# Performance work log

Hardware: AMD Instinct MI355X
Metric: run time of the kernel (lower is better)

The kernel has to match this reference:

```python
import jax, jax.numpy as jnp
import numpy as np

NUM_CLASSES = 20
MEM_SIZE = 512      # memory_bank_size
MAX_VIEWS = 512
TEMP = 0.1
MOMENTUM = 0.999
IGNORE_IDX = 255
AUX_IDX = 254
EPS = 1e-12


def _nearest_resize(gt, Ho, Wo):
    # torch F.interpolate(mode='nearest'): src = floor(dst * in/out)
    B, Hi, Wi = gt.shape
    ri = (jnp.arange(Ho) * Hi) // Ho
    ci = (jnp.arange(Wo) * Wi) // Wo
    return gt[:, ri][:, :, ci]


def _norm_flat(p):
    # L2-normalize over channels, then [B, C, H, W] -> [B, H*W, C]
    p = p / jnp.maximum(jnp.linalg.norm(p, axis=1, keepdims=True), EPS)
    B, C = p.shape[0], p.shape[1]
    return p.reshape(B, C, -1).transpose(0, 2, 1)


def setup_inputs() -> dict:
    key = jax.random.key(0)
    k1, k2, k3, k4, k5 = jax.random.split(key, 5)
    B, D, H, W = 4, 256, 128, 128
    Hg, Wg = 512, 512
    return {
        'main_proj': jax.random.normal(k1, (B, D, H, W), dtype=jnp.float32),
        'main_gt': jax.random.randint(k2, (B, Hg, Wg), 0, NUM_CLASSES).astype(jnp.int64),
        'aux_proj': jax.random.normal(k3, (B, D, H, W), dtype=jnp.float32),
        'aux_gt': jax.random.randint(k4, (B, Hg, Wg), 0, NUM_CLASSES).astype(jnp.int64),
        'memory_bank': jax.random.normal(k5, (NUM_CLASSES, MEM_SIZE, D), dtype=jnp.float32),
    }


def reference(main_proj, main_gt, aux_proj, aux_gt, memory_bank):
    C, M, D = memory_bank.shape
    B, _, H, W = main_proj.shape
    mg = _nearest_resize(main_gt, H, W)
    ag = _nearest_resize(aux_gt, aux_proj.shape[2], aux_proj.shape[3])

    embd = jnp.concatenate([_norm_flat(main_proj), _norm_flat(aux_proj)], axis=1)
    embd = embd.reshape(-1, D)                       # [N, D]
    label = jnp.concatenate([mg.reshape(B, -1), ag.reshape(B, -1)], axis=1).reshape(-1)

    valid = label != IGNORE_IDX
    label = jnp.where(label == AUX_IDX, C - 1, label)

    # per-class gather: stable argsort puts class-c pixels first (deterministic
    # stand-in for torch.randperm selection)
    masks = (label[None, :] == jnp.arange(C)[:, None]) & valid[None, :]   # [C, N]
    counts = masks.sum(axis=1)                                           # [C]
    order = jnp.argsort(~masks, axis=1, stable=True)[:, :M]              # [C, M]
    sel = embd[order]                                                    # [C, M, D]
    sel_valid = jnp.arange(M)[None, :] < counts[:, None]                 # [C, M]

    # momentum scatter-update to memory bank (no grad through features)
    upd = MOMENTUM * memory_bank + (1.0 - MOMENTUM) * jax.lax.stop_gradient(sel)
    upd = upd / jnp.maximum(jnp.linalg.norm(upd, axis=2, keepdims=True), EPS)
    bank = jnp.where(sel_valid[..., None], upd, memory_bank)             # [C, M, D]

    # anchors from current batch (with grad)
    V = min(MAX_VIEWS, M)
    anchors = sel[:, :V].reshape(C * V, D)
    a_valid = sel_valid[:, :V].reshape(-1)
    a_lbl = jnp.repeat(jnp.arange(C), V)

    # contrastive samples from updated bank (constant w.r.t. grad)
    contras = bank.reshape(C * M, D)
    c_valid = jnp.linalg.norm(bank, axis=2).reshape(-1) > 0
    c_lbl = jnp.repeat(jnp.arange(C), M)

    # InfoNCE with masked softmax over valid contrastive columns
    scores = (anchors @ contras.T) / TEMP                                # [A, K]
    scores = jnp.where(c_valid[None, :], scores, -1e9)
    logp = jax.nn.log_softmax(scores, axis=1)
    pos = ((a_lbl[:, None] == c_lbl[None, :]) & c_valid[None, :]).astype(scores.dtype)
    pos_sum = (pos * logp).sum(axis=1)
    pos_cnt = pos.sum(axis=1)
    va = (pos_cnt > 0) & a_valid
    mlpp = jnp.where(va, pos_sum / jnp.maximum(pos_cnt, 1.0), 0.0)
    loss = -mlpp.sum() / jnp.maximum(va.sum(), 1).astype(scores.dtype)
    return loss
```

## Files before the change

### kernel.cpp

```cpp
#include <hip/hip_runtime.h>
#include <cstdint>
#include <math.h>

#define NCLS  20
#define MSZ   512
#define DIM   256
#define HW    16384
#define NPIX  131072
#define AROWS 10240
#define TEMP_INV 10.0f
#define EXP2K 14.4269504088896f

typedef __attribute__((ext_vector_type(8))) short bf16x8;
typedef __attribute__((ext_vector_type(4))) float f32x4;

__device__ __forceinline__ short f2bf(float f) {
    unsigned u = __float_as_uint(f);
    unsigned r = (u + 0x7FFFu + ((u >> 16) & 1u)) >> 16;
    return (short)r;
}
__device__ __forceinline__ float bf2f(short s) {
    return __uint_as_float(((unsigned)(unsigned short)s) << 16);
}
__device__ __forceinline__ float fexp2(float x) {
    float r;
    asm volatile("v_exp_f32 %0, %1" : "=v"(r) : "v"(x));
    return r;
}
__device__ __forceinline__ void gld16(const void* g, void* l) {
    __builtin_amdgcn_global_load_lds(
        (const __attribute__((address_space(1))) unsigned int*)(uintptr_t)g,
        (__attribute__((address_space(3))) unsigned int*)(unsigned int)(uintptr_t)l,
        16, 0, 0);
}

#define ZREG_FLOATS 15488

__global__ __launch_bounds__(256) void k_hist(const int* __restrict__ mg,
                                              const int* __restrict__ ag,
                                              int* __restrict__ labels,
                                              int* __restrict__ hist,
                                              int* __restrict__ pix2row,
                                              float* __restrict__ zreg) {
    int chunk = blockIdx.x, t = threadIdx.x;
    int lane = t & 63;
    int gi = chunk * 256 + t;
    if (gi < ZREG_FLOATS) zreg[gi] = 0.0f;

    int n = gi;
    int b = n >> 15, r = n & 32767;
    const int* g = (r < HW) ? mg : ag;
    int p = (r < HW) ? r : (r - HW);
    int h = p >> 7, w = p & 127;
    int lab = g[(((size_t)b * 512) + (size_t)(h << 2)) * 512 + (size_t)(w << 2)];
    if (lab == 255) lab = -1;
    else if (lab == 254) lab = NCLS - 1;
    labels[n] = lab;
    pix2row[n] = -1;

    __shared__ int cnt20[NCLS];
    if (t < NCLS) cnt20[t] = 0;
    __syncthreads();
#pragma unroll
    for (int c = 0; c < NCLS; ++c) {
        unsigned long long m = __ballot(lab == c);
        if (lane == 0 && m) atomicAdd(&cnt20[c], __popcll(m));
    }
    __syncthreads();
    if (t < NCLS) hist[t * 512 + chunk] = cnt20[t];
}

__global__ __launch_bounds__(256) void k_write(const int* __restrict__ labels,
                                               const int* __restrict__ hist,
                                               int* __restrict__ pix2row,
                                               int* __restrict__ counts) {
    int chunk = blockIdx.x, t = threadIdx.x;
    int lane = t & 63, wv = t >> 6;
    __shared__ int cbase[NCLS];
    __shared__ int wcnt2[4][NCLS];

#pragma unroll
    for (int cc = 0; cc < 5; ++cc) {
        int c = wv * 5 + cc;
        int s = 0;
        for (int j = lane; j < chunk; j += 64) s += hist[c * 512 + j];
#pragma unroll
        for (int o = 32; o > 0; o >>= 1) s += __shfl_down(s, o, 64);
        if (lane == 0) cbase[c] = s;
    }

    int n = chunk * 256 + t;
    int lab = labels[n];
    int myrank = 0;
#pragma unroll
    for (int c = 0; c < NCLS; ++c) {
        unsigned long long m = __ballot(lab == c);
        if (lane == 0) wcnt2[wv][c] = __popcll(m);
        if (lab == c) myrank = __popcll(m & ((1ull << lane) - 1ull));
    }
    __syncthreads();
    if (lab >= 0) {
        int base = cbase[lab] + myrank;
        for (int w = 0; w < wv; ++w) base += wcnt2[w][lab];
        if (base < MSZ) pix2row[n] = lab * MSZ + base;
    }
    if (chunk == 511 && t < NCLS)
        counts[t] = cbase[t] + wcnt2[0][t] + wcnt2[1][t] + wcnt2[2][t] + wcnt2[3][t];
}

__global__ __launch_bounds__(256) void k_scatter(const float* __restrict__ mainp,
                                                 const float* __restrict__ auxp,
                                                 const int* __restrict__ pix2row,
                                                 float* __restrict__ xF) {
    int idx = blockIdx.x * 256 + threadIdx.x;
    int p4 = idx & 4095;
    int ch = (idx >> 12) & 255;
    int bs = idx >> 20;
    int b = bs >> 1, src = bs & 1;
    const float* base = (src ? auxp : mainp) + (size_t)b * DIM * HW + (size_t)ch * HW;
    float4 v = *(const float4*)(base + p4 * 4);
    int4 pr = *(const int4*)(pix2row + bs * HW + p4 * 4);
    if (pr.x >= 0) xF[(size_t)pr.x * DIM + ch] = v.x;
    if (pr.y >= 0) xF[(size_t)pr.y * DIM + ch] = v.y;
    if (pr.z >= 0) xF[(size_t)pr.z * DIM + ch] = v.z;
    if (pr.w >= 0) xF[(size_t)pr.w * DIM + ch] = v.w;
}

__global__ __launch_bounds__(256) void k_nbc(const float* __restrict__ xF,
                                             const float* __restrict__ bank,
                                             const int* __restrict__ counts,
                                             short* __restrict__ anchorsB,
                                             short* __restrict__ contrasB,
                                             int* __restrict__ c_valid,
                                             float* __restrict__ S,
                                             int* __restrict__ pcnt) {
    int blk = blockIdx.x;
    int c = blk >> 3;
    int t = threadIdx.x, lane = t & 63, wv = t >> 6;
    int cc = counts[c];
    int base = blk * 64;
    float sacc[4] = {0.f, 0.f, 0.f, 0.f};
    int vcnt = 0;

    for (int it = 0; it < 16; ++it) {
        int a = base + it * 4 + wv;
        int m = a & 511;
        float4 xv = *(const float4*)&xF[(size_t)a * DIM + lane * 4];
        float x[4] = {xv.x, xv.y, xv.z, xv.w};
        float ss = x[0]*x[0] + x[1]*x[1] + x[2]*x[2] + x[3]*x[3];
#pragma unroll
        for (int o = 1; o < 64; o <<= 1) ss += __shfl_xor(ss, o, 64);
        float scale = 1.0f / fmaxf(sqrtf(ss), 1e-12f);
        float ax[4];
#pragma unroll
        for (int q = 0; q < 4; ++q) ax[q] = x[q] * scale;
        short4 oa;
        oa.x = f2bf(ax[0]); oa.y = f2bf(ax[1]); oa.z = f2bf(ax[2]); oa.w = f2bf(ax[3]);
        *(short4*)&anchorsB[(size_t)a * DIM + lane * 4] = oa;

        bool upd = m < cc;
        float4 bv = *(const float4*)&bank[(size_t)a * DIM + lane * 4];
        float u[4];
        u[0] = upd ? 0.999f * bv.x + 0.001f * ax[0] : bv.x;
        u[1] = upd ? 0.999f * bv.y + 0.001f * ax[1] : bv.y;
        u[2] = upd ? 0.999f * bv.z + 0.001f * ax[2] : bv.z;
        u[3] = upd ? 0.999f * bv.w + 0.001f * ax[3] : bv.w;
        float ss2 = u[0]*u[0] + u[1]*u[1] + u[2]*u[2] + u[3]*u[3];
#pragma unroll
        for (int o = 1; o < 64; o <<= 1) ss2 += __shfl_xor(ss2, o, 64);
        float nrm = sqrtf(ss2);
        float inv = 1.0f / fmaxf(nrm, 1e-12f);
        short oc[4];
        oc[0] = f2bf(upd ? u[0] * inv : bv.x);
        oc[1] = f2bf(upd ? u[1] * inv : bv.y);
        oc[2] = f2bf(upd ? u[2] * inv : bv.z);
        oc[3] = f2bf(upd ? u[3] * inv : bv.w);
        *(short4*)&contrasB[(size_t)a * DIM + lane * 4] = *(short4*)oc;
        bool valid = nrm > 0.0f;
        if (lane == 0) {
            c_valid[a] = valid ? 1 : 0;
            vcnt += valid ? 1 : 0;
        }
        if (valid) {
#pragma unroll
            for (int q = 0; q < 4; ++q) sacc[q] += bf2f(oc[q]);
        }
    }

    __shared__ float s4[4][DIM];
    __shared__ int pv[4];
#pragma unroll
    for (int q = 0; q < 4; ++q) s4[wv][lane * 4 + q] = sacc[q];
    if (lane == 0) pv[wv] = vcnt;
    __syncthreads();
    float s = s4[0][t] + s4[1][t] + s4[2][t] + s4[3][t];
    atomicAdd(&S[c * DIM + t], s);
    if (t == 0) atomicAdd(&pcnt[c], pv[0] + pv[1] + pv[2] + pv[3]);
}

__global__ __launch_bounds__(512, 4) void k_score(const short* __restrict__ A,
                                                  const short* __restrict__ Bc,
                                                  const int* __restrict__ c_valid,
                                                  float* __restrict__ row_sumexp) {
    __shared__ short As[2][128 * 32];
    __shared__ short Bs[2][256 * 32];
    int t = threadIdx.x;
    int lane = t & 63, wv = t >> 6;
    int wr = wv & 1, wc = wv >> 1;
    int row0 = blockIdx.x * 128, col0 = blockIdx.y * 256;
    int lrow = lane >> 2;
    int gseg = (lane & 3) ^ (lrow & 3);
    int qr = lane >> 4, qc = lane & 15;

    f32x4 acc[4][4] = {};

    const short* Ag = A  + (size_t)row0 * DIM;
    const short* Bg = Bc + (size_t)col0 * DIM;

    auto stage = [&](int buf, int k0) {
        gld16(Ag + (size_t)(wv * 16 + lrow) * DIM + k0 + gseg * 8,
              &As[buf][(wv * 16) * 32]);
        gld16(Bg + (size_t)(wv * 32 + lrow) * DIM + k0 + gseg * 8,
              &Bs[buf][(wv * 32) * 32]);
        gld16(Bg + (size_t)(wv * 32 + 16 + lrow) * DIM + k0 + gseg * 8,
              &Bs[buf][(wv * 32 + 16) * 32]);
    };

    stage(0, 0);
#pragma unroll
    for (int k = 0; k < 8; ++k) {
        int cur = k & 1;
        if (k < 7) {
            stage(cur ^ 1, (k + 1) * 32);
            asm volatile("s_waitcnt vmcnt(3)" ::: "memory");
        } else {
            asm volatile("s_waitcnt vmcnt(0)" ::: "memory");
        }
        asm volatile("s_barrier" ::: "memory");

        bf16x8 af[4], bfv[4];
        int slot = (qr ^ (qc & 3)) * 8;
#pragma unroll
        for (int i = 0; i < 4; ++i)
            af[i] = *(const bf16x8*)&As[cur][(wr * 64 + i * 16 + qc) * 32 + slot];
#pragma unroll
        for (int j = 0; j < 4; ++j)
            bfv[j] = *(const bf16x8*)&Bs[cur][(wc * 64 + j * 16 + qc) * 32 + slot];
#pragma unroll
        for (int i = 0; i < 4; ++i)
#pragma unroll
            for (int j = 0; j < 4; ++j)
                acc[i][j] = __builtin_amdgcn_mfma_f32_16x16x32_bf16(af[i], bfv[j], acc[i][j], 0, 0, 0);

        if (k < 7) asm volatile("s_barrier" ::: "memory");
    }

    float cm[4];
#pragma unroll
    for (int j = 0; j < 4; ++j)
        cm[j] = c_valid[col0 + wc * 64 + j * 16 + qc] ? 1.0f : 0.0f;
#pragma unroll
    for (int i = 0; i < 4; ++i)
#pragma unroll
        for (int r = 0; r < 4; ++r) {
            float e = cm[0] * fexp2(acc[i][0][r] * EXP2K)
                    + cm[1] * fexp2(acc[i][1][r] * EXP2K)
                    + cm[2] * fexp2(acc[i][2][r] * EXP2K)
                    + cm[3] * fexp2(acc[i][3][r] * EXP2K);
#pragma unroll
            for (int o = 1; o < 16; o <<= 1) e += __shfl_xor(e, o, 64);
            if (qc == 0)
                atomicAdd(&row_sumexp[row0 + wr * 64 + i * 16 + qr * 4 + r], e);
        }
}

__global__ __launch_bounds__(256) void k_fin(const short* __restrict__ anchorsB,
                                             const float* __restrict__ S,
                                             const int* __restrict__ counts,
                                             const int* __restrict__ pcnt,
                                             const float* __restrict__ row_sumexp,
                                             float* __restrict__ facc,
                                             int* __restrict__ done_cnt,
                                             float* __restrict__ out) {
    int blk = blockIdx.x;
    int c = blk >> 3;
    int t = threadIdx.x, lane = t & 63, wv = t >> 6;
    int pc = pcnt[c], cc = counts[c];
    float lsum = 0.0f, vc = 0.0f;

    for (int it = 0; it < 16; ++it) {
        int a = blk * 64 + it * 4 + wv;
        short4 a4 = *(const short4*)&anchorsB[(size_t)a * DIM + lane * 4];
        float4 s4 = *(const float4*)&S[c * DIM + lane * 4];
        float dot = bf2f(a4.x) * s4.x + bf2f(a4.y) * s4.y
                  + bf2f(a4.z) * s4.z + bf2f(a4.w) * s4.w;
#pragma unroll
        for (int o = 1; o < 64; o <<= 1) dot += __shfl_xor(dot, o, 64);
        if (lane == 0 && (a & 511) < cc && pc > 0) {
            float lse = logf(row_sumexp[a]);
            lsum += (TEMP_INV * dot - (float)pc * lse) / (float)pc;
            vc += 1.0f;
        }
    }

    __shared__ float wls[4], wvc[4];
    if (lane == 0) { wls[wv] = lsum; wvc[wv] = vc; }
    __syncthreads();
    if (t == 0) {
        atomicAdd(&facc[0], wls[0] + wls[1] + wls[2] + wls[3]);
        atomicAdd(&facc[1], wvc[0] + wvc[1] + wvc[2] + wvc[3]);
        __threadfence();
        unsigned d = atomicAdd((unsigned*)done_cnt, 1u);
        if (d == 159u) {
            __threadfence();
            float L = atomicAdd(&facc[0], 0.0f);
            float V = atomicAdd(&facc[1], 0.0f);
            out[0] = -L / fmaxf(V, 1.0f);
        }
    }
}

extern "C" void kernel_launch(void* const* d_in, const int* in_sizes, int n_in,
                              void* d_out, int out_size, void* d_ws, size_t ws_size,
                              hipStream_t stream) {
    const float* main_proj = (const float*)d_in[0];
    const int*   main_gt   = (const int*)d_in[1];
    const float* aux_proj  = (const float*)d_in[2];
    const int*   aux_gt    = (const int*)d_in[3];
    const float* bank      = (const float*)d_in[4];
    float* out = (float*)d_out;

    char* ws = (char*)d_ws;
    int*   labels     = (int*)ws;
    int*   hist       = (int*)(ws + 524288);
    int*   pix2row    = (int*)(ws + 565248);
    int*   c_valid    = (int*)(ws + 1089536);
    float* zreg       = (float*)(ws + 1130496);
    float* row_sumexp = zreg;
    float* S          = zreg + 10240;
    int*   pcnt       = (int*)(zreg + 15360);
    float* facc       = zreg + 15380;
    int*   done_cnt   = (int*)(zreg + 15382);
    int*   counts     = (int*)(ws + 1192448);
    float* xF         = (float*)(ws + 1192704);
    short* anchorsB   = (short*)(ws + 11678464);
    short* contrasB   = (short*)(ws + 16921344);

    k_hist<<<512, 256, 0, stream>>>(main_gt, aux_gt, labels, hist, pix2row, zreg);
    k_write<<<512, 256, 0, stream>>>(labels, hist, pix2row, counts);
    k_scatter<<<32768, 256, 0, stream>>>(main_proj, aux_proj, pix2row, xF);
    k_nbc<<<AROWS / 64, 256, 0, stream>>>(xF, bank, counts, anchorsB, contrasB,
                                          c_valid, S, pcnt);
    dim3 grid(AROWS / 128, AROWS / 256);
    k_score<<<grid, 512, 0, stream>>>(anchorsB, contrasB, c_valid, row_sumexp);
    k_fin<<<AROWS / 64, 256, 0, stream>>>(anchorsB, S, counts, pcnt, row_sumexp,
                                          facc, done_cnt, out);
}
```

Measured before the change: 298.1 us.

## Enlarge score GEMM tile to 256x256 with K=64 stages and ping-pong MFMA scheduling

The score kernel now computes 256x256 output tiles per block instead of 128x256, stages 64-wide K slices (4 iterations instead of 8) into a larger double-buffered LDS with an 8-way XOR swizzle, and splits the MFMA work into four barrier-separated quadrants with s_setprio raised around them. The aim is more data reuse per LDS load, fewer barriers and global loads per FLOP, and better overlap of LDS reads with MFMA. In exchange the grid halves to 1600 blocks, LDS per block grows to 128 KB, occupancy drops, and the extra barriers may add serialization.

```diff
diff --git a/kernel.cpp b/kernel.cpp
--- a/kernel.cpp
+++ b/kernel.cpp
@@ -198,80 +198,111 @@
     if (t == 0) atomicAdd(&pcnt[c], pv[0] + pv[1] + pv[2] + pv[3]);
 }
 
-__global__ __launch_bounds__(512, 4) void k_score(const short* __restrict__ A,
+__global__ __launch_bounds__(512, 2) void k_score(const short* __restrict__ A,
                                                   const short* __restrict__ Bc,
                                                   const int* __restrict__ c_valid,
                                                   float* __restrict__ row_sumexp) {
-    __shared__ short As[2][128 * 32];
-    __shared__ short Bs[2][256 * 32];
-    int t = threadIdx.x;
-    int lane = t & 63, wv = t >> 6;
-    int wr = wv & 1, wc = wv >> 1;
-    int row0 = blockIdx.x * 128, col0 = blockIdx.y * 256;
-    int lrow = lane >> 2;
-    int gseg = (lane & 3) ^ (lrow & 3);
-    int qr = lane >> 4, qc = lane & 15;
-
-    f32x4 acc[4][4] = {};
-
+    __shared__ short lds[2][2][256 * 64];
+    const int t = threadIdx.x;
+    const int lane = t & 63, wv = t >> 6;
+    const int wr = wv & 1, wc = wv >> 1;
+    const int qr = lane >> 4, qc = lane & 15;
+    const int s7 = qc & 7;
+    const int row0 = blockIdx.x * 256, col0 = blockIdx.y * 256;
+
+    const int rl = t >> 3;
+    const int sdat = (t & 7) ^ (rl & 7);
     const short* Ag = A  + (size_t)row0 * DIM;
     const short* Bg = Bc + (size_t)col0 * DIM;
 
-    auto stage = [&](int buf, int k0) {
-        gld16(Ag + (size_t)(wv * 16 + lrow) * DIM + k0 + gseg * 8,
-              &As[buf][(wv * 16) * 32]);
-        gld16(Bg + (size_t)(wv * 32 + lrow) * DIM + k0 + gseg * 8,
-              &Bs[buf][(wv * 32) * 32]);
-        gld16(Bg + (size_t)(wv * 32 + 16 + lrow) * DIM + k0 + gseg * 8,
-              &Bs[buf][(wv * 32 + 16) * 32]);
+    const int sl0 = ((0 + qr) ^ s7) * 8;
+    const int sl1 = ((4 + qr) ^ s7) * 8;
+
+    f32x4 acc[2][2][4][2] = {};
+    bf16x8 A0[4][2], A1[4][2], Bf[2][2];
+
+    auto stage = [&](int buf, int kt) {
+#pragma unroll
+        for (int q = 0; q < 4; ++q)
+            gld16(Ag + (size_t)(q * 64 + rl) * DIM + kt * 64 + sdat * 8,
+                  &lds[buf][0][(q * 64 + wv * 8) * 64]);
+#pragma unroll
+        for (int q = 0; q < 4; ++q)
+            gld16(Bg + (size_t)(q * 64 + rl) * DIM + kt * 64 + sdat * 8,
+                  &lds[buf][1][(q * 64 + wv * 8) * 64]);
     };
+    auto readA = [&](bf16x8 (&Af)[4][2], const short* base, int rh) {
+#pragma unroll
+        for (int rt = 0; rt < 4; ++rt) {
+            const int rb = (wr * 128 + rh * 64 + rt * 16 + qc) * 64;
+            Af[rt][0] = *(const bf16x8*)&base[rb + sl0];
+            Af[rt][1] = *(const bf16x8*)&base[rb + sl1];
+        }
+    };
+    auto readB = [&](const short* base, int ch) {
+#pragma unroll
+        for (int ct = 0; ct < 2; ++ct) {
+            const int rb = (wc * 64 + ch * 32 + ct * 16 + qc) * 64;
+            Bf[ct][0] = *(const bf16x8*)&base[rb + sl0];
+            Bf[ct][1] = *(const bf16x8*)&base[rb + sl1];
+        }
+    };
+
+#define BARR asm volatile("s_barrier" ::: "memory")
+#define DOMFMA(RH, CH, AF)                                                               \
+    _Pragma("unroll")                                                                    \
+    for (int rt = 0; rt < 4; ++rt) {                                                     \
+        _Pragma("unroll")                                                                \
+        for (int ct = 0; ct < 2; ++ct) {                                                 \
+            acc[RH][CH][rt][ct] = __builtin_amdgcn_mfma_f32_16x16x32_bf16(               \
+                AF[rt][0], Bf[ct][0], acc[RH][CH][rt][ct], 0, 0, 0);                     \
+            acc[RH][CH][rt][ct] = __builtin_amdgcn_mfma_f32_16x16x32_bf16(               \
+                AF[rt][1], Bf[ct][1], acc[RH][CH][rt][ct], 0, 0, 0);                     \
+        }                                                                                \
+    }
 
     stage(0, 0);
 #pragma unroll
-    for (int k = 0; k < 8; ++k) {
-        int cur = k & 1;
-        if (k < 7) {
-            stage(cur ^ 1, (k + 1) * 32);
-            asm volatile("s_waitcnt vmcnt(3)" ::: "memory");
-        } else {
-            asm volatile("s_waitcnt vmcnt(0)" ::: "memory");
-        }
-        asm volatile("s_barrier" ::: "memory");
-
-        bf16x8 af[4], bfv[4];
-        int slot = (qr ^ (qc & 3)) * 8;
-#pragma unroll
-        for (int i = 0; i < 4; ++i)
-            af[i] = *(const bf16x8*)&As[cur][(wr * 64 + i * 16 + qc) * 32 + slot];
-#pragma unroll
-        for (int j = 0; j < 4; ++j)
-            bfv[j] = *(const bf16x8*)&Bs[cur][(wc * 64 + j * 16 + qc) * 32 + slot];
-#pragma unroll
-        for (int i = 0; i < 4; ++i)
-#pragma unroll
-            for (int j = 0; j < 4; ++j)
-                acc[i][j] = __builtin_amdgcn_mfma_f32_16x16x32_bf16(af[i], bfv[j], acc[i][j], 0, 0, 0);
-
-        if (k < 7) asm volatile("s_barrier" ::: "memory");
-    }
-
-    float cm[4];
-#pragma unroll
-    for (int j = 0; j < 4; ++j)
-        cm[j] = c_valid[col0 + wc * 64 + j * 16 + qc] ? 1.0f : 0.0f;
-#pragma unroll
-    for (int i = 0; i < 4; ++i)
-#pragma unroll
-        for (int r = 0; r < 4; ++r) {
-            float e = cm[0] * fexp2(acc[i][0][r] * EXP2K)
-                    + cm[1] * fexp2(acc[i][1][r] * EXP2K)
-                    + cm[2] * fexp2(acc[i][2][r] * EXP2K)
-                    + cm[3] * fexp2(acc[i][3][r] * EXP2K);
-#pragma unroll
-            for (int o = 1; o < 16; o <<= 1) e += __shfl_xor(e, o, 64);
-            if (qc == 0)
-                atomicAdd(&row_sumexp[row0 + wr * 64 + i * 16 + qr * 4 + r], e);
-        }
+    for (int kt = 0; kt < 4; ++kt) {
+        const int buf = kt & 1;
+        asm volatile("s_waitcnt vmcnt(0)" ::: "memory");
+        BARR;
+        if (kt < 3) stage(buf ^ 1, kt + 1);
+        const short* Ab = &lds[buf][0][0];
+        const short* Bb = &lds[buf][1][0];
+        readA(A0, Ab, 0); readB(Bb, 0);
+        BARR; __builtin_amdgcn_s_setprio(1); DOMFMA(0, 0, A0); __builtin_amdgcn_s_setprio(0); BARR;
+        readB(Bb, 1);
+        BARR; __builtin_amdgcn_s_setprio(1); DOMFMA(0, 1, A0); __builtin_amdgcn_s_setprio(0); BARR;
+        readA(A1, Ab, 1);
+        BARR; __builtin_amdgcn_s_setprio(1); DOMFMA(1, 1, A1); __builtin_amdgcn_s_setprio(0); BARR;
+        readB(Bb, 0);
+        BARR; __builtin_amdgcn_s_setprio(1); DOMFMA(1, 0, A1); __builtin_amdgcn_s_setprio(0); BARR;
+    }
+#undef DOMFMA
+#undef BARR
+
+    float cm[2][2];
+#pragma unroll
+    for (int ch = 0; ch < 2; ++ch)
+#pragma unroll
+        for (int ct = 0; ct < 2; ++ct)
+            cm[ch][ct] = c_valid[col0 + wc * 64 + ch * 32 + ct * 16 + qc] ? 1.0f : 0.0f;
+#pragma unroll
+    for (int rh = 0; rh < 2; ++rh)
+#pragma unroll
+        for (int rt = 0; rt < 4; ++rt)
+#pragma unroll
+            for (int r = 0; r < 4; ++r) {
+                float e = cm[0][0] * fexp2(acc[rh][0][rt][0][r] * EXP2K)
+                        + cm[0][1] * fexp2(acc[rh][0][rt][1][r] * EXP2K)
+                        + cm[1][0] * fexp2(acc[rh][1][rt][0][r] * EXP2K)
+                        + cm[1][1] * fexp2(acc[rh][1][rt][1][r] * EXP2K);
+#pragma unroll
+                for (int o = 1; o < 16; o <<= 1) e += __shfl_xor(e, o, 64);
+                if (qc == 0)
+                    atomicAdd(&row_sumexp[row0 + wr * 128 + rh * 64 + rt * 16 + qr * 4 + r], e);
+            }
 }
 
 __global__ __launch_bounds__(256) void k_fin(const short* __restrict__ anchorsB,
@@ -351,7 +382,7 @@
     k_scatter<<<32768, 256, 0, stream>>>(main_proj, aux_proj, pix2row, xF);
     k_nbc<<<AROWS / 64, 256, 0, stream>>>(xF, bank, counts, anchorsB, contrasB,
                                           c_valid, S, pcnt);
-    dim3 grid(AROWS / 128, AROWS / 256);
+    dim3 grid(AROWS / 256, AROWS / 256);
     k_score<<<grid, 512, 0, stream>>>(anchorsB, contrasB, c_valid, row_sumexp);
     k_fin<<<AROWS / 64, 256, 0, stream>>>(anchorsB, S, counts, pcnt, row_sumexp,
                                           facc, done_cnt, out);
```

Result: slower. 320.6 us (+7.5%).

## Restage score GEMM with single K=64 LDS buffer and split-phase prefetch

Applied to the files above, without the earlier changes.

The score GEMM kernel drops the double-buffered K=32 LDS tiles in favour of one K=64 tile per stage with an 8-way XOR swizzle. Each iteration reads both K-halves of the fragments into registers first. It then barriers and issues the next global-to-LDS prefetch while the second half's MFMAs run. This halves the number of K iterations and barriers and reduces LDS footprint, which may raise occupancy. In exchange the load for the next tile overlaps only half of the compute and must fully drain at the start of each iteration.

```diff
diff --git a/kernel.cpp b/kernel.cpp
--- a/kernel.cpp
+++ b/kernel.cpp
@@ -202,75 +202,88 @@
                                                   const short* __restrict__ Bc,
                                                   const int* __restrict__ c_valid,
                                                   float* __restrict__ row_sumexp) {
-    __shared__ short As[2][128 * 32];
-    __shared__ short Bs[2][256 * 32];
-    int t = threadIdx.x;
-    int lane = t & 63, wv = t >> 6;
-    int wr = wv & 1, wc = wv >> 1;
-    int row0 = blockIdx.x * 128, col0 = blockIdx.y * 256;
-    int lrow = lane >> 2;
-    int gseg = (lane & 3) ^ (lrow & 3);
-    int qr = lane >> 4, qc = lane & 15;
-
-    f32x4 acc[4][4] = {};
-
+    __shared__ short As[128 * 64];
+    __shared__ short Bs[256 * 64];
+    const int t = threadIdx.x;
+    const int lane = t & 63, wv = t >> 6;
+    const int wr = wv & 1, wc = wv >> 1;
+    const int qr = lane >> 4, qc = lane & 15;
+    const int s7 = qc & 7;
+    const int row0 = blockIdx.x * 128, col0 = blockIdx.y * 256;
+
+    const int rl8 = t >> 3;
+    const int sdat = (t & 7) ^ (rl8 & 7);
     const short* Ag = A  + (size_t)row0 * DIM;
     const short* Bg = Bc + (size_t)col0 * DIM;
 
-    auto stage = [&](int buf, int k0) {
-        gld16(Ag + (size_t)(wv * 16 + lrow) * DIM + k0 + gseg * 8,
-              &As[buf][(wv * 16) * 32]);
-        gld16(Bg + (size_t)(wv * 32 + lrow) * DIM + k0 + gseg * 8,
-              &Bs[buf][(wv * 32) * 32]);
-        gld16(Bg + (size_t)(wv * 32 + 16 + lrow) * DIM + k0 + gseg * 8,
-              &Bs[buf][(wv * 32 + 16) * 32]);
+    const int sl0 = ((0 + qr) ^ s7) * 8;
+    const int sl1 = ((4 + qr) ^ s7) * 8;
+
+    f32x4 acc[4][4] = {};
+
+    auto stage = [&](int kt) {
+#pragma unroll
+        for (int r = 0; r < 2; ++r)
+            gld16(Ag + (size_t)(r * 64 + rl8) * DIM + kt * 64 + sdat * 8,
+                  &As[(r * 64 + wv * 8) * 64]);
+#pragma unroll
+        for (int r = 0; r < 4; ++r)
+            gld16(Bg + (size_t)(r * 64 + rl8) * DIM + kt * 64 + sdat * 8,
+                  &Bs[(r * 64 + wv * 8) * 64]);
     };
 
-    stage(0, 0);
-#pragma unroll
-    for (int k = 0; k < 8; ++k) {
-        int cur = k & 1;
-        if (k < 7) {
-            stage(cur ^ 1, (k + 1) * 32);
-            asm volatile("s_waitcnt vmcnt(3)" ::: "memory");
-        } else {
-            asm volatile("s_waitcnt vmcnt(0)" ::: "memory");
-        }
+    stage(0);
+    for (int kt = 0; kt < 4; ++kt) {
+        asm volatile("s_waitcnt vmcnt(0)" ::: "memory");
         asm volatile("s_barrier" ::: "memory");
 
-        bf16x8 af[4], bfv[4];
-        int slot = (qr ^ (qc & 3)) * 8;
-#pragma unroll
-        for (int i = 0; i < 4; ++i)
-            af[i] = *(const bf16x8*)&As[cur][(wr * 64 + i * 16 + qc) * 32 + slot];
-#pragma unroll
-        for (int j = 0; j < 4; ++j)
-            bfv[j] = *(const bf16x8*)&Bs[cur][(wc * 64 + j * 16 + qc) * 32 + slot];
-#pragma unroll
-        for (int i = 0; i < 4; ++i)
-#pragma unroll
-            for (int j = 0; j < 4; ++j)
-                acc[i][j] = __builtin_amdgcn_mfma_f32_16x16x32_bf16(af[i], bfv[j], acc[i][j], 0, 0, 0);
-
-        if (k < 7) asm volatile("s_barrier" ::: "memory");
+        bf16x8 a0[4], b0[4], a1[4], b1[4];
+#pragma unroll
+        for (int rt = 0; rt < 4; ++rt)
+            a0[rt] = *(const bf16x8*)&As[(wr * 64 + rt * 16 + qc) * 64 + sl0];
+#pragma unroll
+        for (int ct = 0; ct < 4; ++ct)
+            b0[ct] = *(const bf16x8*)&Bs[(wc * 64 + ct * 16 + qc) * 64 + sl0];
+#pragma unroll
+        for (int rt = 0; rt < 4; ++rt)
+#pragma unroll
+            for (int ct = 0; ct < 4; ++ct)
+                acc[rt][ct] = __builtin_amdgcn_mfma_f32_16x16x32_bf16(a0[rt], b0[ct], acc[rt][ct], 0, 0, 0);
+#pragma unroll
+        for (int rt = 0; rt < 4; ++rt)
+            a1[rt] = *(const bf16x8*)&As[(wr * 64 + rt * 16 + qc) * 64 + sl1];
+#pragma unroll
+        for (int ct = 0; ct < 4; ++ct)
+            b1[ct] = *(const bf16x8*)&Bs[(wc * 64 + ct * 16 + qc) * 64 + sl1];
+
+        asm volatile("s_waitcnt lgkmcnt(0)" ::: "memory");
+        __builtin_amdgcn_sched_barrier(0);
+        asm volatile("s_barrier" ::: "memory");
+        if (kt < 3) stage(kt + 1);
+
+#pragma unroll
+        for (int rt = 0; rt < 4; ++rt)
+#pragma unroll
+            for (int ct = 0; ct < 4; ++ct)
+                acc[rt][ct] = __builtin_amdgcn_mfma_f32_16x16x32_bf16(a1[rt], b1[ct], acc[rt][ct], 0, 0, 0);
     }
 
     float cm[4];
 #pragma unroll
-    for (int j = 0; j < 4; ++j)
-        cm[j] = c_valid[col0 + wc * 64 + j * 16 + qc] ? 1.0f : 0.0f;
-#pragma unroll
-    for (int i = 0; i < 4; ++i)
+    for (int ct = 0; ct < 4; ++ct)
+        cm[ct] = c_valid[col0 + wc * 64 + ct * 16 + qc] ? 1.0f : 0.0f;
+#pragma unroll
+    for (int rt = 0; rt < 4; ++rt)
 #pragma unroll
         for (int r = 0; r < 4; ++r) {
-            float e = cm[0] * fexp2(acc[i][0][r] * EXP2K)
-                    + cm[1] * fexp2(acc[i][1][r] * EXP2K)
-                    + cm[2] * fexp2(acc[i][2][r] * EXP2K)
-                    + cm[3] * fexp2(acc[i][3][r] * EXP2K);
+            float e = cm[0] * fexp2(acc[rt][0][r] * EXP2K)
+                    + cm[1] * fexp2(acc[rt][1][r] * EXP2K)
+                    + cm[2] * fexp2(acc[rt][2][r] * EXP2K)
+                    + cm[3] * fexp2(acc[rt][3][r] * EXP2K);
 #pragma unroll
             for (int o = 1; o < 16; o <<= 1) e += __shfl_xor(e, o, 64);
             if (qc == 0)
-                atomicAdd(&row_sumexp[row0 + wr * 64 + i * 16 + qr * 4 + r], e);
+                atomicAdd(&row_sumexp[row0 + wr * 64 + rt * 16 + qr * 4 + r], e);
         }
 }
 
```

Result: no change. 297.8 us (-0.1%).
